# Performance work log

Hardware: AMD Instinct MI355X
Metric: run time of the kernel (lower is better)

The kernel has to match this reference:

```python
import jax, jax.numpy as jnp
import numpy as np
from jax import lax

EPS = 1e-12


def _conv_block(x, w, scale, bias, pool):
    # x: (N, Cin, H, W), w: (Cout, Cin, 3, 3). BN in eval mode folded into scale/bias.
    y = lax.conv_general_dilated(x, w, window_strides=(1, 1), padding='SAME',
                                 dimension_numbers=('NCHW', 'OIHW', 'NCHW'))
    y = y * scale[None, :, None, None] + bias[None, :, None, None]
    y = jax.nn.relu(y)
    if pool:
        y = lax.reduce_window(y, -jnp.inf, lax.max, (1, 1, 2, 2), (1, 1, 2, 2), 'VALID')
    return y


def _encoder(x, w1, s1, b1, w2, s2, b2, w3, s3, b3, w4, s4, b4):
    x = _conv_block(x, w1, s1, b1, True)
    x = _conv_block(x, w2, s2, b2, True)
    x = _conv_block(x, w3, s3, b3, False)
    x = _conv_block(x, w4, s4, b4, False)
    return x  # (N, 64, 21, 21)


def _l2norm(x, axis):
    n = jnp.sqrt(jnp.sum(x * x, axis=axis, keepdims=True))
    return x / jnp.maximum(n, EPS)


def setup_inputs() -> dict:
    key = jax.random.key(0)
    ks = jax.random.split(key, 8)
    B, NQ, Way, Shot, C, H, W = 2, 75, 5, 5, 3, 84, 84
    D = 64
    inp = {
        'query': jax.random.normal(ks[0], (B, NQ, C, H, W), jnp.float32),
        'support': jax.random.normal(ks[1], (B, Way, Shot, C, H, W), jnp.float32),
        'w1': jax.random.normal(ks[2], (D, C, 3, 3), jnp.float32) * 0.1,
        'w2': jax.random.normal(ks[3], (D, D, 3, 3), jnp.float32) * 0.05,
        'w3': jax.random.normal(ks[4], (D, D, 3, 3), jnp.float32) * 0.05,
        'w4': jax.random.normal(ks[5], (D, D, 3, 3), jnp.float32) * 0.05,
    }
    for i in range(1, 5):
        inp[f's{i}'] = jnp.ones((D,), jnp.float32)
        inp[f'b{i}'] = jnp.zeros((D,), jnp.float32)
    return inp


def reference(query, support, w1, s1, b1, w2, s2, b2, w3, s3, b3, w4, s4, b4):
    B, NQ, C, H, W = query.shape
    _, Way, Shot, _, _, _ = support.shape
    q_flat = query.reshape(B * NQ, C, H, W)
    s_flat = support.reshape(B * Way * Shot, C, H, W)
    q_feat = _encoder(q_flat, w1, s1, b1, w2, s2, b2, w3, s3, b3, w4, s4, b4)
    s_feat = _encoder(s_flat, w1, s1, b1, w2, s2, b2, w3, s3, b3, w4, s4, b4)
    D, h, w = q_feat.shape[1], q_feat.shape[2], q_feat.shape[3]
    HW = h * w
    q_local = _l2norm(q_feat.reshape(B, NQ, D, HW), axis=2)            # (B,NQ,D,HW)
    s_local = s_feat.reshape(B, Way, Shot, D, HW).mean(axis=2)          # mean over shots
    s_local = _l2norm(s_local, axis=2)                                  # (B,Way,D,HW)
    # all pairwise local cosine similarities, batched in one einsum
    sim = jnp.einsum('bqdm,bcdn->bqcmn', q_local, s_local)              # (B,NQ,Way,HW,HW)
    best = sim.max(axis=-1)                                             # best match per query descriptor
    scores = best.mean(axis=-1)                                         # (B,NQ,Way)
    return scores.reshape(B * NQ, Way)
```

## Files before the change

### kernel.cpp

```cpp
#include <hip/hip_runtime.h>

#define EPS 1e-12f

#define NIMG   200
#define NQIMG  150
#define BDIM   2
#define NQ     75
#define WAY    5
#define SHOT   5
#define DCH    64
#define H1     84
#define H2     42
#define H3     21
#define HW1    7056
#define HW2    1764
#define HW3    441
#define PH     86
#define PSZ    7396
#define SST    448

#define PAD_BLKS  17335
#define W1_BLKS   8
#define W_BLKS    432

typedef __attribute__((ext_vector_type(8))) short bf16x8;
typedef __attribute__((ext_vector_type(4))) float f32x4;

__device__ __forceinline__ unsigned short f2bf(float f) {
    unsigned u = __float_as_uint(f);
    u += 0x7fffu + ((u >> 16) & 1u);
    return (unsigned short)(u >> 16);
}
__device__ __forceinline__ float bf2f(unsigned short h) {
    return __uint_as_float(((unsigned)h) << 16);
}
__device__ __forceinline__ int swz(int pix, int c) {
    return pix * 128 + ((c ^ ((pix >> 1) & 7)) << 4);
}

__global__ __launch_bounds__(256) void prep(
    const float* __restrict__ qin, const float* __restrict__ sin_,
    const float* __restrict__ w1, const float* __restrict__ s1,
    const float* __restrict__ w2, const float* __restrict__ s2,
    const float* __restrict__ w3, const float* __restrict__ s3,
    const float* __restrict__ w4, const float* __restrict__ s4,
    unsigned short* __restrict__ pad, unsigned short* __restrict__ p1,
    unsigned short* __restrict__ p2, unsigned short* __restrict__ p3,
    unsigned short* __restrict__ p4)
{
    int blk = blockIdx.x;
    if (blk < PAD_BLKS) {
        int idx = blk * 256 + threadIdx.x;
        if (idx >= NIMG * 3 * PSZ) return;
        int img = idx / (3 * PSZ);
        int rem = idx % (3 * PSZ);
        int ci = rem / PSZ, p = rem % PSZ;
        int iy = p / PH, ix = p % PH;
        float v = 0.f;
        if (iy >= 1 && iy <= H1 && ix >= 1 && ix <= H1) {
            const float* src = (img < NQIMG) ? (qin + (size_t)img * 3 * HW1)
                                             : (sin_ + (size_t)(img - NQIMG) * 3 * HW1);
            v = src[(size_t)ci * HW1 + (iy - 1) * H1 + (ix - 1)];
        }
        pad[idx] = f2bf(v);
    } else if (blk < PAD_BLKS + W1_BLKS) {
        int idx = (blk - PAD_BLKS) * 256 + threadIdx.x;
        int j = idx & 7, lane = (idx >> 3) & 63, mt = idx >> 9;
        int co = (mt << 4) + (lane & 15);
        int k = ((lane >> 4) << 3) + j;
        float v = 0.f;
        if (k < 27) {
            int ci = k / 9, s = k % 9;
            v = w1[(co * 3 + ci) * 9 + s] * s1[co];
        }
        p1[idx] = f2bf(v);
    } else {
        int idx = (blk - PAD_BLKS - W1_BLKS) * 256 + threadIdx.x;
        int which = idx / 36864;
        int r = idx % 36864;
        int j = r & 7, lane = (r >> 3) & 63, mt = (r >> 9) & 3, t = (r >> 11) & 1, s = r >> 12;
        int co = (mt << 4) + (lane & 15);
        int ci = (t << 5) + ((lane >> 4) << 3) + j;
        const float* w = (which == 0) ? w2 : (which == 1) ? w3 : w4;
        const float* sc = (which == 0) ? s2 : (which == 1) ? s3 : s4;
        unsigned short* p = (which == 0) ? p2 : (which == 1) ? p3 : p4;
        p[r] = f2bf(w[(co * 64 + ci) * 9 + s] * sc[co]);
    }
}

__global__ __launch_bounds__(256) void conv12_fused(
    const unsigned short* __restrict__ pad,
    const unsigned short* __restrict__ wp1, const float* __restrict__ bias1,
    const unsigned short* __restrict__ wp2, const float* __restrict__ bias2,
    unsigned short* __restrict__ out)
{
    int img = blockIdx.x / 7, tg = blockIdx.x % 7;
    int tid = threadIdx.x;
    __shared__ __attribute__((aligned(16))) unsigned short strip[3 * 18 * 86];
    __shared__ unsigned short lds2[352 * DCH];

    const unsigned* srcd = (const unsigned*)pad;
    size_t ibase = (size_t)img * 3 * (PSZ / 2);
    #pragma unroll
    for (int it = 0; it < 10; it++) {
        int i = it * 256 + tid;
        if (i < 2322) {
            int ci = i / 774, rem = i % 774;
            int sr = rem / 43, d = rem % 43;
            int y = 12 * tg - 3 + sr;
            unsigned v = 0;
            if (y >= -1 && y <= 84)
                v = srcd[ibase + ci * 3698 + (y + 1) * 43 + d];
            ((unsigned*)strip)[ci * 774 + sr * 43 + d] = v;
        }
    }
    __syncthreads();

    int wv = tid >> 6, lane = tid & 63;
    int lc = lane & 15, kg = lane >> 4;

    {
        const bf16x8* w1v = (const bf16x8*)wp1;
        bf16x8 a0 = w1v[lane];
        bf16x8 a1 = w1v[64 + lane];
        bf16x8 a2 = w1v[128 + lane];
        bf16x8 a3 = w1v[192 + lane];

        int off[8];
        #pragma unroll
        for (int j = 0; j < 8; j++) {
            int k = (kg << 3) + j;
            int kk = k < 27 ? k : 0;
            int ci = kk / 9, s = kk % 9;
            off[j] = ci * 1548 + (s / 3) * 86 + (s % 3);
        }

        f32x4 bini[4];
        #pragma unroll
        for (int mt = 0; mt < 4; mt++) {
            float4 bq = *reinterpret_cast<const float4*>(bias1 + (mt << 4) + (kg << 2));
            bini[mt] = (f32x4){bq.x, bq.y, bq.z, bq.w};
        }

        #pragma unroll
        for (int rnd = 0; rnd < 6; rnd++) {
            int pl = rnd * 64 + wv * 16 + lc;
            bool instrip = pl < 352;
            int plc = instrip ? pl : 0;
            int rr = plc / 44, cc = plc % 44;
            int pr = 6 * tg - 1 + rr, pc = cc - 1;
            bool validpx = instrip && ((unsigned)pr < (unsigned)H2) && ((unsigned)pc < (unsigned)H2);
            int ccc = ((unsigned)pc < (unsigned)H2) ? cc : 1;
            int base = (2 * rr) * 86 + (2 * ccc - 2);

            bf16x8 b[4];
            #pragma unroll
            for (int j = 0; j < 8; j++) {
                int a = base + off[j];
                b[0][j] = (short)strip[a];
                b[1][j] = (short)strip[a + 1];
                b[2][j] = (short)strip[a + 86];
                b[3][j] = (short)strip[a + 87];
            }

            f32x4 acc[4][4];
            #pragma unroll
            for (int mt = 0; mt < 4; mt++)
                #pragma unroll
                for (int sub = 0; sub < 4; sub++)
                    acc[mt][sub] = bini[mt];
            #pragma unroll
            for (int sub = 0; sub < 4; sub++) {
                acc[0][sub] = __builtin_amdgcn_mfma_f32_16x16x32_bf16(a0, b[sub], acc[0][sub], 0, 0, 0);
                acc[1][sub] = __builtin_amdgcn_mfma_f32_16x16x32_bf16(a1, b[sub], acc[1][sub], 0, 0, 0);
                acc[2][sub] = __builtin_amdgcn_mfma_f32_16x16x32_bf16(a2, b[sub], acc[2][sub], 0, 0, 0);
                acc[3][sub] = __builtin_amdgcn_mfma_f32_16x16x32_bf16(a3, b[sub], acc[3][sub], 0, 0, 0);
            }

            if (instrip) {
                #pragma unroll
                for (int mt = 0; mt < 4; mt++) {
                    uint2 pk = make_uint2(0u, 0u);
                    if (validpx) {
                        unsigned short uo[4];
                        #pragma unroll
                        for (int r = 0; r < 4; r++) {
                            float m = fmaxf(fmaxf(acc[mt][0][r], acc[mt][1][r]),
                                            fmaxf(acc[mt][2][r], acc[mt][3][r]));
                            uo[r] = f2bf(fmaxf(m, 0.f));
                        }
                        pk.x = (unsigned)uo[0] | ((unsigned)uo[1] << 16);
                        pk.y = (unsigned)uo[2] | ((unsigned)uo[3] << 16);
                    }
                    int c = (mt << 1) + (kg >> 1);
                    *(uint2*)((char*)lds2 + swz(pl, c) + ((kg & 1) << 3)) = pk;
                }
            }
        }
    }
    __syncthreads();

    int p_local = wv * 16 + lc;
    bool valid = p_local < 63;
    int pl = valid ? p_local : 62;
    int pyl = pl / 21, pxl = pl % 21;
    int pixc[4];
    #pragma unroll
    for (int sub = 0; sub < 4; sub++)
        pixc[sub] = (2 * pyl + (sub >> 1) + 1) * 44 + (2 * pxl + (sub & 1) + 1);

    f32x4 bini[4];
    #pragma unroll
    for (int mt = 0; mt < 4; mt++) {
        float4 bq = *reinterpret_cast<const float4*>(bias2 + (mt << 4) + (kg << 2));
        bini[mt] = (f32x4){bq.x, bq.y, bq.z, bq.w};
    }

    const bf16x8* wvv = (const bf16x8*)wp2;
    f32x4 acc[4][4];
    #pragma unroll
    for (int i = 0; i < 4; i++)
        #pragma unroll
        for (int j = 0; j < 4; j++)
            acc[i][j] = bini[i];

    for (int s = 0; s < 9; s++) {
        int offs = (s / 3 - 1) * 44 + (s % 3 - 1);
        #pragma unroll
        for (int t = 0; t < 2; t++) {
            int fbase = ((s * 2 + t) * 4) << 6;
            bf16x8 a0 = wvv[fbase + lane];
            bf16x8 a1 = wvv[fbase + 64 + lane];
            bf16x8 a2 = wvv[fbase + 128 + lane];
            bf16x8 a3 = wvv[fbase + 192 + lane];
            int c = (t << 2) + kg;
            bf16x8 b[4];
            #pragma unroll
            for (int sub = 0; sub < 4; sub++) {
                int pix = pixc[sub] + offs;
                b[sub] = *(const bf16x8*)((const char*)lds2 + swz(pix, c));
            }
            #pragma unroll
            for (int sub = 0; sub < 4; sub++) {
                acc[0][sub] = __builtin_amdgcn_mfma_f32_16x16x32_bf16(a0, b[sub], acc[0][sub], 0, 0, 0);
                acc[1][sub] = __builtin_amdgcn_mfma_f32_16x16x32_bf16(a1, b[sub], acc[1][sub], 0, 0, 0);
                acc[2][sub] = __builtin_amdgcn_mfma_f32_16x16x32_bf16(a2, b[sub], acc[2][sub], 0, 0, 0);
                acc[3][sub] = __builtin_amdgcn_mfma_f32_16x16x32_bf16(a3, b[sub], acc[3][sub], 0, 0, 0);
            }
        }
    }

    if (!valid) return;
    int p = tg * 63 + p_local;
    #pragma unroll
    for (int mt = 0; mt < 4; mt++) {
        unsigned short uo[4];
        #pragma unroll
        for (int r = 0; r < 4; r++) {
            float m = fmaxf(fmaxf(acc[mt][0][r], acc[mt][1][r]),
                            fmaxf(acc[mt][2][r], acc[mt][3][r]));
            uo[r] = f2bf(fmaxf(m, 0.f));
        }
        uint2 pk;
        pk.x = (unsigned)uo[0] | ((unsigned)uo[1] << 16);
        pk.y = (unsigned)uo[2] | ((unsigned)uo[3] << 16);
        *reinterpret_cast<uint2*>(out + ((size_t)img * HW3 + p) * DCH + (mt << 4) + (kg << 2)) = pk;
    }
}

__global__ __launch_bounds__(256) void conv34_fused(
    const unsigned short* __restrict__ act,
    const unsigned short* __restrict__ wp3, const unsigned short* __restrict__ wp4,
    const float* __restrict__ b3, const float* __restrict__ b4,
    unsigned short* __restrict__ a4out,
    unsigned short* __restrict__ qlout)
{
    int img = blockIdx.x;
    int tid = threadIdx.x;
    __shared__ unsigned short lds[529 * DCH];

    const unsigned short* ab = act + (size_t)img * HW3 * DCH;
    #pragma unroll
    for (int it = 0; it < 17; it++) {
        int idx = it * 256 + tid;
        if (idx < 529 * 8) {
            int pix = idx >> 3, c = idx & 7;
            int r = pix / 23, xx = pix % 23;
            int y = r - 1, x = xx - 1;
            bf16x8 v = (bf16x8)(short)0;
            if ((unsigned)y < (unsigned)H3 && (unsigned)x < (unsigned)H3)
                v = *(const bf16x8*)(ab + ((size_t)(y * H3 + x)) * DCH + (c << 3));
            *(bf16x8*)((char*)lds + swz(pix, c)) = v;
        }
    }
    __syncthreads();

    int wv = tid >> 6, lane = tid & 63;
    int lc = lane & 15, kg = lane >> 4;
    int pixBase[7];
    bool pv[7];
    #pragma unroll
    for (int i = 0; i < 7; i++) {
        int p = (wv * 7 + i) * 16 + lc;
        pv[i] = p < HW3;
        int pc = pv[i] ? p : HW3 - 1;
        pixBase[i] = (pc / 21) * 23 + (pc % 21);
    }

    f32x4 bini[4];
    #pragma unroll
    for (int mt = 0; mt < 4; mt++) {
        float4 bq = *reinterpret_cast<const float4*>(b3 + (mt << 4) + (kg << 2));
        bini[mt] = (f32x4){bq.x, bq.y, bq.z, bq.w};
    }

    f32x4 acc[7][4];
    #pragma unroll
    for (int i = 0; i < 7; i++)
        #pragma unroll
        for (int m = 0; m < 4; m++)
            acc[i][m] = bini[m];

    const bf16x8* wv3 = (const bf16x8*)wp3;
    for (int s = 0; s < 9; s++) {
        int offs = (s / 3) * 23 + (s % 3);
        #pragma unroll
        for (int t = 0; t < 2; t++) {
            int fbase = ((s * 2 + t) * 4) << 6;
            bf16x8 a0 = wv3[fbase + lane];
            bf16x8 a1 = wv3[fbase + 64 + lane];
            bf16x8 a2 = wv3[fbase + 128 + lane];
            bf16x8 a3 = wv3[fbase + 192 + lane];
            int c = (t << 2) + kg;
            #pragma unroll
            for (int i = 0; i < 7; i++) {
                int pix = pixBase[i] + offs;
                bf16x8 bb = *(const bf16x8*)((const char*)lds + swz(pix, c));
                acc[i][0] = __builtin_amdgcn_mfma_f32_16x16x32_bf16(a0, bb, acc[i][0], 0, 0, 0);
                acc[i][1] = __builtin_amdgcn_mfma_f32_16x16x32_bf16(a1, bb, acc[i][1], 0, 0, 0);
                acc[i][2] = __builtin_amdgcn_mfma_f32_16x16x32_bf16(a2, bb, acc[i][2], 0, 0, 0);
                acc[i][3] = __builtin_amdgcn_mfma_f32_16x16x32_bf16(a3, bb, acc[i][3], 0, 0, 0);
            }
        }
    }

    __syncthreads();

    #pragma unroll
    for (int i = 0; i < 7; i++) {
        if (!pv[i]) continue;
        int pix = pixBase[i] + 24;
        #pragma unroll
        for (int mt = 0; mt < 4; mt++) {
            unsigned short uo[4];
            #pragma unroll
            for (int r = 0; r < 4; r++)
                uo[r] = f2bf(fmaxf(acc[i][mt][r], 0.f));
            uint2 pk;
            pk.x = (unsigned)uo[0] | ((unsigned)uo[1] << 16);
            pk.y = (unsigned)uo[2] | ((unsigned)uo[3] << 16);
            int c = (mt << 1) + (kg >> 1);
            *(uint2*)((char*)lds + swz(pix, c) + ((kg & 1) << 3)) = pk;
        }
    }
    #pragma unroll
    for (int it = 0; it < 3; it++) {
        int idx = it * 256 + tid;
        if (idx < 704) {
            int j = idx >> 3, c = idx & 7;
            int pix;
            if (j < 23)      pix = j;
            else if (j < 46) pix = 506 + (j - 23);
            else { int k = j - 46; pix = (1 + (k >> 1)) * 23 + (k & 1) * 22; }
            *(bf16x8*)((char*)lds + swz(pix, c)) = (bf16x8)(short)0;
        }
    }
    __syncthreads();

    #pragma unroll
    for (int mt = 0; mt < 4; mt++) {
        float4 bq = *reinterpret_cast<const float4*>(b4 + (mt << 4) + (kg << 2));
        bini[mt] = (f32x4){bq.x, bq.y, bq.z, bq.w};
    }
    #pragma unroll
    for (int i = 0; i < 7; i++)
        #pragma unroll
        for (int m = 0; m < 4; m++)
            acc[i][m] = bini[m];

    const bf16x8* wv4 = (const bf16x8*)wp4;
    for (int s = 0; s < 9; s++) {
        int offs = (s / 3) * 23 + (s % 3);
        #pragma unroll
        for (int t = 0; t < 2; t++) {
            int fbase = ((s * 2 + t) * 4) << 6;
            bf16x8 a0 = wv4[fbase + lane];
            bf16x8 a1 = wv4[fbase + 64 + lane];
            bf16x8 a2 = wv4[fbase + 128 + lane];
            bf16x8 a3 = wv4[fbase + 192 + lane];
            int c = (t << 2) + kg;
            #pragma unroll
            for (int i = 0; i < 7; i++) {
                int pix = pixBase[i] + offs;
                bf16x8 bb = *(const bf16x8*)((const char*)lds + swz(pix, c));
                acc[i][0] = __builtin_amdgcn_mfma_f32_16x16x32_bf16(a0, bb, acc[i][0], 0, 0, 0);
                acc[i][1] = __builtin_amdgcn_mfma_f32_16x16x32_bf16(a1, bb, acc[i][1], 0, 0, 0);
                acc[i][2] = __builtin_amdgcn_mfma_f32_16x16x32_bf16(a2, bb, acc[i][2], 0, 0, 0);
                acc[i][3] = __builtin_amdgcn_mfma_f32_16x16x32_bf16(a3, bb, acc[i][3], 0, 0, 0);
            }
        }
    }

    if (img < NQIMG) {
        #pragma unroll
        for (int i = 0; i < 7; i++) {
            float v[4][4];
            float ssq = 0.f;
            #pragma unroll
            for (int mt = 0; mt < 4; mt++)
                #pragma unroll
                for (int r = 0; r < 4; r++) {
                    float x = fmaxf(acc[i][mt][r], 0.f);
                    v[mt][r] = x;
                    ssq = fmaf(x, x, ssq);
                }
            ssq += __shfl_xor(ssq, 16, 64);
            ssq += __shfl_xor(ssq, 32, 64);
            float inv = 1.f / fmaxf(sqrtf(ssq), EPS);
            if (!pv[i]) continue;
            int p = (wv * 7 + i) * 16 + lc;
            #pragma unroll
            for (int mt = 0; mt < 4; mt++) {
                unsigned short uo[4];
                #pragma unroll
                for (int r = 0; r < 4; r++)
                    uo[r] = f2bf(v[mt][r] * inv);
                uint2 pk;
                pk.x = (unsigned)uo[0] | ((unsigned)uo[1] << 16);
                pk.y = (unsigned)uo[2] | ((unsigned)uo[3] << 16);
                *reinterpret_cast<uint2*>(qlout + ((size_t)img * HW3 + p) * DCH + (mt << 4) + (kg << 2)) = pk;
            }
        }
    } else {
        #pragma unroll
        for (int mt = 0; mt < 4; mt++) {
            #pragma unroll
            for (int i = 0; i < 7; i++) {
                if (!pv[i]) continue;
                int p = (wv * 7 + i) * 16 + lc;
                unsigned short uo[4];
                #pragma unroll
                for (int r = 0; r < 4; r++)
                    uo[r] = f2bf(fmaxf(acc[i][mt][r], 0.f));
                uint2 pk;
                pk.x = (unsigned)uo[0] | ((unsigned)uo[1] << 16);
                pk.y = (unsigned)uo[2] | ((unsigned)uo[3] << 16);
                *reinterpret_cast<uint2*>(a4out + ((size_t)img * HW3 + p) * DCH + (mt << 4) + (kg << 2)) = pk;
            }
        }
    }
}

__global__ __launch_bounds__(256) void s_mean_norm(
    const unsigned short* __restrict__ feat, unsigned short* __restrict__ s_local)
{
    int idx = blockIdx.x * 256 + threadIdx.x;
    if (idx >= BDIM * WAY * SST) return;
    int hw = idx % SST;
    int bc = idx / SST;
    bf16x8* o = (bf16x8*)(s_local + (size_t)idx * DCH);
    if (hw >= HW3) {
        #pragma unroll
        for (int g = 0; g < 8; g++) o[g] = (bf16x8)(short)0;
        return;
    }
    int img0 = NQIMG + bc * SHOT;
    float v[DCH];
    #pragma unroll
    for (int d = 0; d < DCH; d++) v[d] = 0.f;
    for (int sh = 0; sh < SHOT; sh++) {
        const bf16x8* f = (const bf16x8*)(feat + ((size_t)(img0 + sh) * HW3 + hw) * DCH);
        #pragma unroll
        for (int g = 0; g < 8; g++) {
            bf16x8 x = f[g];
            #pragma unroll
            for (int j = 0; j < 8; j++)
                v[g * 8 + j] += bf2f((unsigned short)x[j]);
        }
    }
    float ss = 0.f;
    #pragma unroll
    for (int d = 0; d < DCH; d++) {
        v[d] *= (1.f / SHOT);
        ss = fmaf(v[d], v[d], ss);
    }
    float inv = 1.f / fmaxf(sqrtf(ss), EPS);
    #pragma unroll
    for (int g = 0; g < 8; g++) {
        bf16x8 pk;
        #pragma unroll
        for (int j = 0; j < 8; j++) pk[j] = (short)f2bf(v[g * 8 + j] * inv);
        o[g] = pk;
    }
}

__global__ __launch_bounds__(256) void sim_mfma(
    const unsigned short* __restrict__ qloc,
    const unsigned short* __restrict__ sloc,
    float* __restrict__ out)
{
    int blk = blockIdx.x;
    int imgq = blk / WAY, way = blk % WAY;
    int b = imgq / NQ;
    const unsigned short* qp = qloc + (size_t)imgq * HW3 * DCH;
    const unsigned short* sp = sloc + (size_t)(b * WAY + way) * SST * DCH;

    int tid = threadIdx.x;
    int wv = tid >> 6, lane = tid & 63;
    int lc = lane & 15, kg = lane >> 4;
    int mt0 = wv * 7;

    bf16x8 qa0[7], qa1[7];
    #pragma unroll
    for (int i = 0; i < 7; i++) {
        const unsigned short* qrow = qp + (size_t)((mt0 + i) * 16 + lc) * DCH + (kg << 3);
        qa0[i] = *(const bf16x8*)(qrow);
        qa1[i] = *(const bf16x8*)(qrow + 32);
    }
    f32x4 rmax[7];
    #pragma unroll
    for (int i = 0; i < 7; i++)
        rmax[i] = (f32x4){-1e30f, -1e30f, -1e30f, -1e30f};

    const f32x4 z4 = (f32x4){0.f, 0.f, 0.f, 0.f};
    const unsigned short* sbase = sp + (size_t)lc * DCH + (kg << 3);

    for (int g = 0; g < 6; g++) {
        bf16x8 s0[4], s1[4];
        #pragma unroll
        for (int u = 0; u < 4; u++) {
            const unsigned short* r0 = sbase + (size_t)(4 * g + u) * 16 * DCH;
            s0[u] = *(const bf16x8*)(r0);
            s1[u] = *(const bf16x8*)(r0 + 32);
        }
        #pragma unroll
        for (int i = 0; i < 7; i++) {
            f32x4 a[4];
            #pragma unroll
            for (int u = 0; u < 4; u++) {
                a[u] = __builtin_amdgcn_mfma_f32_16x16x32_bf16(qa0[i], s0[u], z4, 0, 0, 0);
                a[u] = __builtin_amdgcn_mfma_f32_16x16x32_bf16(qa1[i], s1[u], a[u], 0, 0, 0);
            }
            #pragma unroll
            for (int r = 0; r < 4; r++)
                rmax[i][r] = fmaxf(rmax[i][r],
                                   fmaxf(fmaxf(a[0][r], a[1][r]), fmaxf(a[2][r], a[3][r])));
        }
    }
    {
        bf16x8 s0[4], s1[4];
        #pragma unroll
        for (int u = 0; u < 4; u++) {
            const unsigned short* r0 = sbase + (size_t)(24 + u) * 16 * DCH;
            s0[u] = *(const bf16x8*)(r0);
            s1[u] = *(const bf16x8*)(r0 + 32);
        }
        bool nval = (432 + lc) < HW3;
        #pragma unroll
        for (int i = 0; i < 7; i++) {
            f32x4 a[4];
            #pragma unroll
            for (int u = 0; u < 4; u++) {
                a[u] = __builtin_amdgcn_mfma_f32_16x16x32_bf16(qa0[i], s0[u], z4, 0, 0, 0);
                a[u] = __builtin_amdgcn_mfma_f32_16x16x32_bf16(qa1[i], s1[u], a[u], 0, 0, 0);
            }
            #pragma unroll
            for (int r = 0; r < 4; r++)
                rmax[i][r] = fmaxf(rmax[i][r],
                                   fmaxf(fmaxf(a[0][r], a[1][r]),
                                         fmaxf(a[2][r], nval ? a[3][r] : -1e30f)));
        }
    }

    float msum = 0.f;
    #pragma unroll
    for (int i = 0; i < 7; i++) {
        #pragma unroll
        for (int r = 0; r < 4; r++) {
            float v = rmax[i][r];
            v = fmaxf(v, __shfl_xor(v, 1, 64));
            v = fmaxf(v, __shfl_xor(v, 2, 64));
            v = fmaxf(v, __shfl_xor(v, 4, 64));
            v = fmaxf(v, __shfl_xor(v, 8, 64));
            int m = (mt0 + i) * 16 + (kg << 2) + r;
            if (lc == 0 && m < HW3) msum += v;
        }
    }
    #pragma unroll
    for (int off = 32; off > 0; off >>= 1)
        msum += __shfl_xor(msum, off, 64);
    __shared__ float red[4];
    if (lane == 0) red[wv] = msum;
    __syncthreads();
    if (tid == 0)
        out[(size_t)imgq * WAY + way] = (red[0] + red[1] + red[2] + red[3]) * (1.f / HW3);
}

extern "C" void kernel_launch(void* const* d_in, const int* in_sizes, int n_in,
                              void* d_out, int out_size, void* d_ws, size_t ws_size,
                              hipStream_t stream) {
    const float* query   = (const float*)d_in[0];
    const float* support = (const float*)d_in[1];
    const float* w1 = (const float*)d_in[2];
    const float* w2 = (const float*)d_in[3];
    const float* w3 = (const float*)d_in[4];
    const float* w4 = (const float*)d_in[5];
    const float* s1 = (const float*)d_in[6];
    const float* b1 = (const float*)d_in[7];
    const float* s2 = (const float*)d_in[8];
    const float* b2 = (const float*)d_in[9];
    const float* s3 = (const float*)d_in[10];
    const float* b3 = (const float*)d_in[11];
    const float* s4 = (const float*)d_in[12];
    const float* b4 = (const float*)d_in[13];
    float* out = (float*)d_out;

    char* ws = (char*)d_ws;
    unsigned short* A2  = (unsigned short*)(ws);
    unsigned short* A4  = (unsigned short*)(ws + 11289600);
    unsigned short* QL  = (unsigned short*)(ws + 22579200);
    unsigned short* SL  = (unsigned short*)(ws + 31046400);
    unsigned short* WP2 = (unsigned short*)(ws + 31619840);
    unsigned short* WP3 = (unsigned short*)(ws + 31693568);
    unsigned short* WP4 = (unsigned short*)(ws + 31767296);
    unsigned short* WP1 = (unsigned short*)(ws + 31841024);
    unsigned short* PAD = (unsigned short*)(ws + 31845120);

    prep<<<PAD_BLKS + W1_BLKS + W_BLKS, 256, 0, stream>>>(
        query, support, w1, s1, w2, s2, w3, s3, w4, s4, PAD, WP1, WP2, WP3, WP4);

    conv12_fused<<<NIMG * 7, 256, 0, stream>>>(PAD, WP1, b1, WP2, b2, A2);
    conv34_fused<<<NIMG, 256, 0, stream>>>(A2, WP3, WP4, b3, b4, A4, QL);

    s_mean_norm<<<(BDIM * WAY * SST + 255) / 256, 256, 0, stream>>>(A4, SL);

    sim_mfma<<<NQIMG * WAY, 256, 0, stream>>>(QL, SL, out);
}
```

Baseline: 139.9 us.

## Recast conv1 as 4x4 window with shifted weights to vectorize strip loads

Measured after the change: 173.7 us. 24.2% more time.

```diff
diff --git a/kernel.cpp b/kernel.cpp
--- a/kernel.cpp
+++ b/kernel.cpp
@@ -20,11 +20,12 @@
 #define SST    448
 
 #define PAD_BLKS  17335
-#define W1_BLKS   8
+#define W1_BLKS   64
 #define W_BLKS    432
 
 typedef __attribute__((ext_vector_type(8))) short bf16x8;
 typedef __attribute__((ext_vector_type(4))) float f32x4;
+typedef __attribute__((ext_vector_type(4))) unsigned u32x4;
 
 __device__ __forceinline__ unsigned short f2bf(float f) {
     unsigned u = __float_as_uint(f);
@@ -65,14 +66,15 @@
         pad[idx] = f2bf(v);
     } else if (blk < PAD_BLKS + W1_BLKS) {
         int idx = (blk - PAD_BLKS) * 256 + threadIdx.x;
-        int j = idx & 7, lane = (idx >> 3) & 63, mt = idx >> 9;
-        int co = (mt << 4) + (lane & 15);
-        int k = ((lane >> 4) << 3) + j;
+        int j = idx & 7, lane = (idx >> 3) & 63;
+        int mt = (idx >> 9) & 3, sub = (idx >> 11) & 3, half = (idx >> 13) & 1;
+        int kg = lane >> 4, lr = lane & 15;
+        int co = (mt << 4) + lr;
+        int r = (half << 1) + (j >> 2), c = j & 3;
+        int ky = r - (sub >> 1), kx = c - (sub & 1);
         float v = 0.f;
-        if (k < 27) {
-            int ci = k / 9, s = k % 9;
-            v = w1[(co * 3 + ci) * 9 + s] * s1[co];
-        }
+        if (kg < 3 && ky >= 0 && ky < 3 && kx >= 0 && kx < 3)
+            v = w1[(co * 3 + kg) * 9 + ky * 3 + kx] * s1[co];
         p1[idx] = f2bf(v);
     } else {
         int idx = (blk - PAD_BLKS - W1_BLKS) * 256 + threadIdx.x;
@@ -121,19 +123,16 @@
 
     {
         const bf16x8* w1v = (const bf16x8*)wp1;
-        bf16x8 a0 = w1v[lane];
-        bf16x8 a1 = w1v[64 + lane];
-        bf16x8 a2 = w1v[128 + lane];
-        bf16x8 a3 = w1v[192 + lane];
-
-        int off[8];
-        #pragma unroll
-        for (int j = 0; j < 8; j++) {
-            int k = (kg << 3) + j;
-            int kk = k < 27 ? k : 0;
-            int ci = kk / 9, s = kk % 9;
-            off[j] = ci * 1548 + (s / 3) * 86 + (s % 3);
-        }
+        bf16x8 A[2][4][4];
+        #pragma unroll
+        for (int half = 0; half < 2; half++)
+            #pragma unroll
+            for (int sub = 0; sub < 4; sub++)
+                #pragma unroll
+                for (int mt = 0; mt < 4; mt++)
+                    A[half][sub][mt] = w1v[(((half * 4 + sub) * 4) + mt) * 64 + lane];
+
+        int ci = kg < 3 ? kg : 2;
 
         f32x4 bini[4];
         #pragma unroll
@@ -151,17 +150,18 @@
             int pr = 6 * tg - 1 + rr, pc = cc - 1;
             bool validpx = instrip && ((unsigned)pr < (unsigned)H2) && ((unsigned)pc < (unsigned)H2);
             int ccc = ((unsigned)pc < (unsigned)H2) ? cc : 1;
-            int base = (2 * rr) * 86 + (2 * ccc - 2);
-
-            bf16x8 b[4];
-            #pragma unroll
-            for (int j = 0; j < 8; j++) {
-                int a = base + off[j];
-                b[0][j] = (short)strip[a];
-                b[1][j] = (short)strip[a + 1];
-                b[2][j] = (short)strip[a + 86];
-                b[3][j] = (short)strip[a + 87];
-            }
+            int pbyte = (ci * 1548 + (2 * rr) * 86 + (2 * ccc - 2)) * 2;
+
+            unsigned p[4][2];
+            #pragma unroll
+            for (int r = 0; r < 4; r++) {
+                p[r][0] = *(const unsigned*)((const char*)strip + pbyte + r * 172);
+                p[r][1] = *(const unsigned*)((const char*)strip + pbyte + r * 172 + 4);
+            }
+            u32x4 t0 = (u32x4){p[0][0], p[0][1], p[1][0], p[1][1]};
+            u32x4 t1 = (u32x4){p[2][0], p[2][1], p[3][0], p[3][1]};
+            bf16x8 B0 = *(bf16x8*)&t0;
+            bf16x8 B1 = *(bf16x8*)&t1;
 
             f32x4 acc[4][4];
             #pragma unroll
@@ -170,12 +170,12 @@
                 for (int sub = 0; sub < 4; sub++)
                     acc[mt][sub] = bini[mt];
             #pragma unroll
-            for (int sub = 0; sub < 4; sub++) {
-                acc[0][sub] = __builtin_amdgcn_mfma_f32_16x16x32_bf16(a0, b[sub], acc[0][sub], 0, 0, 0);
-                acc[1][sub] = __builtin_amdgcn_mfma_f32_16x16x32_bf16(a1, b[sub], acc[1][sub], 0, 0, 0);
-                acc[2][sub] = __builtin_amdgcn_mfma_f32_16x16x32_bf16(a2, b[sub], acc[2][sub], 0, 0, 0);
-                acc[3][sub] = __builtin_amdgcn_mfma_f32_16x16x32_bf16(a3, b[sub], acc[3][sub], 0, 0, 0);
-            }
+            for (int sub = 0; sub < 4; sub++)
+                #pragma unroll
+                for (int mt = 0; mt < 4; mt++) {
+                    acc[mt][sub] = __builtin_amdgcn_mfma_f32_16x16x32_bf16(A[0][sub][mt], B0, acc[mt][sub], 0, 0, 0);
+                    acc[mt][sub] = __builtin_amdgcn_mfma_f32_16x16x32_bf16(A[1][sub][mt], B1, acc[mt][sub], 0, 0, 0);
+                }
 
             if (instrip) {
                 #pragma unroll
@@ -634,7 +634,7 @@
     unsigned short* WP3 = (unsigned short*)(ws + 31693568);
     unsigned short* WP4 = (unsigned short*)(ws + 31767296);
     unsigned short* WP1 = (unsigned short*)(ws + 31841024);
-    unsigned short* PAD = (unsigned short*)(ws + 31845120);
+    unsigned short* PAD = (unsigned short*)(ws + 31873792);
 
     prep<<<PAD_BLKS + W1_BLKS + W_BLKS, 256, 0, stream>>>(
         query, support, w1, s1, w2, s2, w3, s3, w4, s4, PAD, WP1, WP2, WP3, WP4);
```

## Stage support descriptors in swizzled LDS for sim kernel; vectorize padding prep

Applied to the files above, without the earlier changes.

Result: faster. 127.8 us (-8.6%).

```diff
diff --git a/kernel.cpp b/kernel.cpp
--- a/kernel.cpp
+++ b/kernel.cpp
@@ -19,7 +19,7 @@
 #define PSZ    7396
 #define SST    448
 
-#define PAD_BLKS  17335
+#define PAD_BLKS  4334
 #define W1_BLKS   8
 #define W_BLKS    432
 
@@ -50,19 +50,28 @@
 {
     int blk = blockIdx.x;
     if (blk < PAD_BLKS) {
-        int idx = blk * 256 + threadIdx.x;
-        if (idx >= NIMG * 3 * PSZ) return;
+        int idx4 = blk * 256 + threadIdx.x;
+        if (idx4 >= NIMG * 3 * PSZ / 4) return;
+        int idx = idx4 * 4;
         int img = idx / (3 * PSZ);
         int rem = idx % (3 * PSZ);
         int ci = rem / PSZ, p = rem % PSZ;
-        int iy = p / PH, ix = p % PH;
-        float v = 0.f;
-        if (iy >= 1 && iy <= H1 && ix >= 1 && ix <= H1) {
-            const float* src = (img < NQIMG) ? (qin + (size_t)img * 3 * HW1)
-                                             : (sin_ + (size_t)(img - NQIMG) * 3 * HW1);
-            v = src[(size_t)ci * HW1 + (iy - 1) * H1 + (ix - 1)];
-        }
-        pad[idx] = f2bf(v);
+        const float* src = (img < NQIMG) ? (qin + (size_t)img * 3 * HW1)
+                                         : (sin_ + (size_t)(img - NQIMG) * 3 * HW1);
+        unsigned short o[4];
+        #pragma unroll
+        for (int e = 0; e < 4; e++) {
+            int pe = p + e;
+            int iy = pe / PH, ix = pe % PH;
+            float v = 0.f;
+            if (iy >= 1 && iy <= H1 && ix >= 1 && ix <= H1)
+                v = src[(size_t)ci * HW1 + (iy - 1) * H1 + (ix - 1)];
+            o[e] = f2bf(v);
+        }
+        uint2 pk;
+        pk.x = (unsigned)o[0] | ((unsigned)o[1] << 16);
+        pk.y = (unsigned)o[2] | ((unsigned)o[3] << 16);
+        *reinterpret_cast<uint2*>(pad + idx) = pk;
     } else if (blk < PAD_BLKS + W1_BLKS) {
         int idx = (blk - PAD_BLKS) * 256 + threadIdx.x;
         int j = idx & 7, lane = (idx >> 3) & 63, mt = idx >> 9;
@@ -515,7 +524,17 @@
     const unsigned short* qp = qloc + (size_t)imgq * HW3 * DCH;
     const unsigned short* sp = sloc + (size_t)(b * WAY + way) * SST * DCH;
 
+    __shared__ unsigned short slds[SST * DCH];
     int tid = threadIdx.x;
+    #pragma unroll
+    for (int it = 0; it < 14; it++) {
+        int idx = it * 256 + tid;
+        int pix = idx >> 3, c = idx & 7;
+        bf16x8 v = *(const bf16x8*)(sp + ((size_t)pix << 6) + (c << 3));
+        *(bf16x8*)((char*)slds + swz(pix, c)) = v;
+    }
+    __syncthreads();
+
     int wv = tid >> 6, lane = tid & 63;
     int lc = lane & 15, kg = lane >> 4;
     int mt0 = wv * 7;
@@ -533,15 +552,15 @@
         rmax[i] = (f32x4){-1e30f, -1e30f, -1e30f, -1e30f};
 
     const f32x4 z4 = (f32x4){0.f, 0.f, 0.f, 0.f};
-    const unsigned short* sbase = sp + (size_t)lc * DCH + (kg << 3);
-
+
+    #pragma unroll
     for (int g = 0; g < 6; g++) {
         bf16x8 s0[4], s1[4];
         #pragma unroll
         for (int u = 0; u < 4; u++) {
-            const unsigned short* r0 = sbase + (size_t)(4 * g + u) * 16 * DCH;
-            s0[u] = *(const bf16x8*)(r0);
-            s1[u] = *(const bf16x8*)(r0 + 32);
+            int pix = (4 * g + u) * 16 + lc;
+            s0[u] = *(const bf16x8*)((const char*)slds + swz(pix, kg));
+            s1[u] = *(const bf16x8*)((const char*)slds + swz(pix, 4 + kg));
         }
         #pragma unroll
         for (int i = 0; i < 7; i++) {
@@ -552,18 +571,19 @@
                 a[u] = __builtin_amdgcn_mfma_f32_16x16x32_bf16(qa1[i], s1[u], a[u], 0, 0, 0);
             }
             #pragma unroll
-            for (int r = 0; r < 4; r++)
-                rmax[i][r] = fmaxf(rmax[i][r],
-                                   fmaxf(fmaxf(a[0][r], a[1][r]), fmaxf(a[2][r], a[3][r])));
+            for (int r = 0; r < 4; r++) {
+                float t = fmaxf(fmaxf(rmax[i][r], a[0][r]), a[1][r]);
+                rmax[i][r] = fmaxf(fmaxf(t, a[2][r]), a[3][r]);
+            }
         }
     }
     {
         bf16x8 s0[4], s1[4];
         #pragma unroll
         for (int u = 0; u < 4; u++) {
-            const unsigned short* r0 = sbase + (size_t)(24 + u) * 16 * DCH;
-            s0[u] = *(const bf16x8*)(r0);
-            s1[u] = *(const bf16x8*)(r0 + 32);
+            int pix = (24 + u) * 16 + lc;
+            s0[u] = *(const bf16x8*)((const char*)slds + swz(pix, kg));
+            s1[u] = *(const bf16x8*)((const char*)slds + swz(pix, 4 + kg));
         }
         bool nval = (432 + lc) < HW3;
         #pragma unroll
@@ -575,10 +595,10 @@
                 a[u] = __builtin_amdgcn_mfma_f32_16x16x32_bf16(qa1[i], s1[u], a[u], 0, 0, 0);
             }
             #pragma unroll
-            for (int r = 0; r < 4; r++)
-                rmax[i][r] = fmaxf(rmax[i][r],
-                                   fmaxf(fmaxf(a[0][r], a[1][r]),
-                                         fmaxf(a[2][r], nval ? a[3][r] : -1e30f)));
+            for (int r = 0; r < 4; r++) {
+                float t = fmaxf(fmaxf(rmax[i][r], a[0][r]), a[1][r]);
+                rmax[i][r] = fmaxf(fmaxf(t, a[2][r]), nval ? a[3][r] : -1e30f);
+            }
         }
     }
 
```
